# Kernel optimization log

Measured on AMD Instinct MI355X. Metric: run time of the kernel, lower is better.

The kernel has to match this reference:

```python
import jax, jax.numpy as jnp
import numpy as np

B, MAX_NODE, MEM_LEN, DIM, HEADS, LAYERS, DEG = 32, 1024, 256, 128, 4, 4, 16
CH = DIM // HEADS


def setup_inputs() -> dict:
    key = jax.random.key(0)
    ks = jax.random.split(key, 16)
    counts = np.array([512 + 16 * i for i in range(B)])  # ragged graph sizes, sum = 24320
    N = int(counts.sum())
    node2batch = np.repeat(np.arange(B), counts)
    node2pos = np.concatenate([np.arange(c) for c in counts])
    bmask = np.arange(MAX_NODE)[None, :] < counts[:, None]
    rng = np.random.default_rng(0)
    srcs, dsts, off = [], [], 0
    for c in counts:  # edges stay within each graph
        srcs.append(off + rng.integers(0, c, size=DEG * c))
        dsts.append(off + rng.integers(0, c, size=DEG * c))
        off += c
    edge_index = np.stack([np.concatenate(srcs), np.concatenate(dsts)])

    def rn(k, shape, scale=0.05):
        return jax.random.normal(k, shape, jnp.float32) * scale

    return dict(
        node_feats=rn(ks[0], (N, DIM), 1.0),
        edge_feats=rn(ks[1], (edge_index.shape[1], DIM), 1.0),
        memory=rn(ks[2], (B, MEM_LEN, DIM), 1.0),
        Wn=rn(ks[3], (LAYERS, DIM, DIM)), bn=jnp.zeros((LAYERS, DIM)),
        We=rn(ks[4], (LAYERS, DIM, DIM)),
        att_src=rn(ks[5], (LAYERS, HEADS, CH)),
        att_dst=rn(ks[6], (LAYERS, HEADS, CH)),
        att_edge=rn(ks[7], (LAYERS, HEADS, CH)),
        ln1_g=jnp.ones((LAYERS, DIM)), ln1_b=jnp.zeros((LAYERS, DIM)),
        ln2_g=jnp.ones((LAYERS, DIM)), ln2_b=jnp.zeros((LAYERS, DIM)),
        Wq=rn(ks[8], (LAYERS, DIM, DIM)), Wk=rn(ks[9], (LAYERS, DIM, DIM)),
        Wv=rn(ks[10], (LAYERS, DIM, DIM)), Wo=rn(ks[11], (LAYERS, DIM, DIM)),
        Ew1=rn(ks[12], (LAYERS, 3 * DIM, DIM)), Eb1=jnp.zeros((LAYERS, DIM)),
        Ew2=rn(ks[13], (LAYERS, DIM, DIM)), Eb2=jnp.zeros((LAYERS, DIM)),
        edge_index=jnp.asarray(edge_index, jnp.int32),
        node2batch=jnp.asarray(node2batch, jnp.int32),
        node2pos=jnp.asarray(node2pos, jnp.int32),
        batch_mask=jnp.asarray(bmask),
        mem_pad_mask=jnp.ones((B, MEM_LEN), bool),
    )


def _ln(x, g, b):
    mu = x.mean(-1, keepdims=True)
    v = ((x - mu) ** 2).mean(-1, keepdims=True)
    return (x - mu) * jax.lax.rsqrt(v + 1e-5) * g + b


def reference(node_feats, edge_feats, memory, Wn, bn, We, att_src, att_dst, att_edge,
              ln1_g, ln1_b, ln2_g, ln2_b, Wq, Wk, Wv, Wo, Ew1, Eb1, Ew2, Eb2,
              edge_index, node2batch, node2pos, batch_mask, mem_pad_mask):
    N = node_feats.shape[0]
    src, dst = edge_index[0], edge_index[1]
    # [B, max_node, mem_len]: attend only valid memory slots from valid nodes
    cross_mask = mem_pad_mask[:, None, :] & batch_mask[:, :, None]
    x, e = node_feats, edge_feats
    for l in range(LAYERS):
        # --- edge-conditioned GAT conv (segment softmax over dst) ---
        h = (x @ Wn[l]).reshape(N, HEADS, CH)
        eh = (e @ We[l]).reshape(-1, HEADS, CH)
        logits = (h[src] * att_src[l]).sum(-1) + (h[dst] * att_dst[l]).sum(-1) + (eh * att_edge[l]).sum(-1)
        logits = jax.nn.leaky_relu(logits, 0.2)  # [E, H]
        m = jax.ops.segment_max(logits, dst, num_segments=N)
        ew = jnp.exp(logits - m[dst])
        den = jax.ops.segment_sum(ew, dst, num_segments=N)
        alpha = ew / (den[dst] + 1e-16)
        conv = jax.ops.segment_sum(alpha[..., None] * (h[src] + eh), dst, num_segments=N)
        conv = conv.reshape(N, DIM) + bn[l]
        x = jax.nn.relu(_ln(conv, ln1_g[l], ln1_b[l])) + x
        # --- graph2batch scatter into dense padded tensor ---
        dense = jnp.zeros((B, MAX_NODE, DIM), x.dtype).at[node2batch, node2pos].set(x)
        # --- cross attention against memory ---
        q = (dense @ Wq[l]).reshape(B, MAX_NODE, HEADS, CH)
        k = (memory @ Wk[l]).reshape(B, MEM_LEN, HEADS, CH)
        v = (memory @ Wv[l]).reshape(B, MEM_LEN, HEADS, CH)
        scores = jnp.einsum('bqhc,bkhc->bhqk', q, k) / np.float32(np.sqrt(CH))
        scores = jnp.where(cross_mask[:, None], scores, jnp.float32(-1e9))
        ao = jnp.einsum('bhqk,bkhc->bqhc', jax.nn.softmax(scores, axis=-1), v)
        ao = ao.reshape(B, MAX_NODE, DIM) @ Wo[l]
        dense = jax.nn.relu(_ln(ao + dense, ln2_g[l], ln2_b[l]))
        x = dense[node2batch, node2pos]  # batch2graph gather
        # --- residual sparse edge update ---
        ecat = jnp.concatenate([e, x[src], x[dst]], axis=-1)
        e = e + jax.nn.relu(ecat @ Ew1[l] + Eb1[l]) @ Ew2[l] + Eb2[l]
    return x, e
```

## Files before the change

kernel.cpp:

```cpp
#include <hip/hip_runtime.h>

#define DIM    128
#define HEADS  4
#define CH     32
#define MEMLEN 256
#define LAYERS 4

typedef unsigned int uint;
typedef unsigned short ushort;
using bf16x8 = __attribute__((ext_vector_type(8))) short;
using f32x4  = __attribute__((ext_vector_type(4))) float;

__device__ __forceinline__ ushort bf16_rn(float x) {
    uint u = __float_as_uint(x);
    uint r = (u + 0x7fffu + ((u >> 16) & 1u)) >> 16;
    return (ushort)r;
}
__device__ __forceinline__ void split_bf(float v, ushort& h, ushort& lo) {
    h = bf16_rn(v);
    float hf = __uint_as_float(((uint)h) << 16);
    lo = bf16_rn(v - hf);
}


__global__ void copy_f4(const float4* __restrict__ in, float4* __restrict__ out, long n) {
    long i = (long)blockIdx.x * blockDim.x + threadIdx.x;
    long stride = (long)gridDim.x * blockDim.x;
    for (; i < n; i += stride) out[i] = in[i];
}

__global__ void hist_k(const int* __restrict__ dst, int E, int* __restrict__ deg) {
    int e = blockIdx.x * blockDim.x + threadIdx.x;
    if (e < E) atomicAdd(&deg[dst[e]], 1);
}

__global__ void csr_offsets(const int* __restrict__ deg, int n, int* __restrict__ off) {
    __shared__ int part[1024];
    int t = threadIdx.x;
    int chunk = (n + 1023) >> 10;
    int lo = t * chunk, hi = min(lo + chunk, n);
    int s = 0;
    for (int i = lo; i < hi; i++) s += deg[i];
    part[t] = s; __syncthreads();
    for (int d = 1; d < 1024; d <<= 1) {
        int v = part[t];
        int add = (t >= d) ? part[t - d] : 0;
        __syncthreads();
        part[t] = v + add;
        __syncthreads();
    }
    int run = (t == 0) ? 0 : part[t - 1];
    for (int i = lo; i < hi; i++) { off[i] = run; run += deg[i]; }
    if (t == 1023) off[n] = part[1023];
}

__global__ void csr_fill(const int* __restrict__ dst, int E, const int* __restrict__ off,
                         int* __restrict__ cur, int* __restrict__ csr) {
    int e = blockIdx.x * blockDim.x + threadIdx.x;
    if (e < E) {
        int d = dst[e];
        int p = atomicAdd(&cur[d], 1);
        csr[off[d] + p] = e;
    }
}

__global__ void make_w1f(const float* __restrict__ Ew1, ushort* __restrict__ W1f) {
    int i = blockIdx.x * 256 + threadIdx.x;
    if (i >= LAYERS * 12 * 8 * 64 * 8) return;
    int l = i / 49152; int r = i % 49152;
    int ks = r / 4096;  int r2 = r % 4096;
    int ct = r2 / 512;  int r3 = r2 % 512;
    int lane = r3 / 8;  int j = r3 % 8;
    int k = ks * 32 + (lane >> 4) * 8 + j;
    int n = (lane & 15) + 16 * ct;
    const float* W = Ew1 + (size_t)l * 3 * DIM * DIM;
    float v = W[(size_t)(k % 128) * DIM + n];
    ushort h = bf16_rn(v);
    ushort out = h;
    if (k >= 256) {
        float hf = __uint_as_float(((uint)h) << 16);
        out = bf16_rn(v - hf);
    }
    W1f[i] = out;
}

__global__ void make_w2f(const float* __restrict__ Ew2, ushort* __restrict__ W2f) {
    int i = blockIdx.x * 256 + threadIdx.x;
    if (i >= LAYERS * 8 * 8 * 64 * 8) return;
    int l = i / 32768; int r = i % 32768;
    int ks = r / 4096;  int r2 = r % 4096;
    int ct = r2 / 512;  int r3 = r2 % 512;
    int lane = r3 / 8;  int j = r3 % 8;
    int k = ks * 32 + (lane >> 4) * 8 + j;
    int n = (lane & 15) + 16 * ct;
    const float* W = Ew2 + (size_t)l * DIM * DIM;
    W2f[i] = bf16_rn(W[(size_t)(k >> 1) * DIM + n]);
}

__global__ __launch_bounds__(256) void gemm128(const float* __restrict__ A,
                                               const float* __restrict__ W,
                                               const float* __restrict__ bias,
                                               float* __restrict__ out, int R) {
    int r0 = blockIdx.x * 64, t = threadIdx.x;
    __shared__ float at[64][DIM];
    for (int i = t; i < 64 * 32; i += 256) {
        int rr = i >> 5, cc = i & 31;
        if (r0 + rr < R)
            ((float4*)at[rr])[cc] = ((const float4*)(A + (size_t)(r0 + rr) * DIM))[cc];
    }
    __syncthreads();
    int c0 = (t & 31) * 4;
    int rb = (t >> 5) * 8;
    float acc[8][4];
#pragma unroll
    for (int ee = 0; ee < 8; ee++)
        acc[ee][0] = acc[ee][1] = acc[ee][2] = acc[ee][3] = 0.f;
    for (int k = 0; k < DIM; k += 4) {
        float4 w0 = *(const float4*)&W[(k + 0) * DIM + c0];
        float4 w1 = *(const float4*)&W[(k + 1) * DIM + c0];
        float4 w2 = *(const float4*)&W[(k + 2) * DIM + c0];
        float4 w3 = *(const float4*)&W[(k + 3) * DIM + c0];
#pragma unroll
        for (int ee = 0; ee < 8; ee++) {
            float4 a = *(float4*)&at[rb + ee][k];
            acc[ee][0] += a.x * w0.x + a.y * w1.x + a.z * w2.x + a.w * w3.x;
            acc[ee][1] += a.x * w0.y + a.y * w1.y + a.z * w2.y + a.w * w3.y;
            acc[ee][2] += a.x * w0.z + a.y * w1.z + a.z * w2.z + a.w * w3.z;
            acc[ee][3] += a.x * w0.w + a.y * w1.w + a.z * w2.w + a.w * w3.w;
        }
    }
    float4 bb = make_float4(0.f, 0.f, 0.f, 0.f);
    if (bias) bb = *(const float4*)&bias[c0];
#pragma unroll
    for (int ee = 0; ee < 8; ee++) {
        int r = r0 + rb + ee;
        if (r < R) {
            float4 o = make_float4(acc[ee][0] + bb.x, acc[ee][1] + bb.y,
                                   acc[ee][2] + bb.z, acc[ee][3] + bb.w);
            *(float4*)&out[(size_t)r * DIM + c0] = o;
        }
    }
}

__global__ __launch_bounds__(256, 2) void gemm128_dual(const float* __restrict__ A,
                                                       const float* __restrict__ Wa,
                                                       const float* __restrict__ Wb,
                                                       const float* __restrict__ biasA,
                                                       float* __restrict__ outA,
                                                       float* __restrict__ outB, int R) {
    int r0 = blockIdx.x * 64, t = threadIdx.x;
    __shared__ float at[64][DIM];
    for (int i = t; i < 64 * 32; i += 256) {
        int rr = i >> 5, cc = i & 31;
        if (r0 + rr < R)
            ((float4*)at[rr])[cc] = ((const float4*)(A + (size_t)(r0 + rr) * DIM))[cc];
    }
    __syncthreads();
    int c0 = (t & 31) * 4;
    int rb = (t >> 5) * 8;
    float accA[8][4], accB[8][4];
#pragma unroll
    for (int ee = 0; ee < 8; ee++)
#pragma unroll
        for (int j = 0; j < 4; j++) { accA[ee][j] = 0.f; accB[ee][j] = 0.f; }
    for (int k = 0; k < DIM; k += 4) {
        float4 wa0 = *(const float4*)&Wa[(k + 0) * DIM + c0];
        float4 wa1 = *(const float4*)&Wa[(k + 1) * DIM + c0];
        float4 wa2 = *(const float4*)&Wa[(k + 2) * DIM + c0];
        float4 wa3 = *(const float4*)&Wa[(k + 3) * DIM + c0];
        float4 wb0 = *(const float4*)&Wb[(k + 0) * DIM + c0];
        float4 wb1 = *(const float4*)&Wb[(k + 1) * DIM + c0];
        float4 wb2 = *(const float4*)&Wb[(k + 2) * DIM + c0];
        float4 wb3 = *(const float4*)&Wb[(k + 3) * DIM + c0];
#pragma unroll
        for (int ee = 0; ee < 8; ee++) {
            float4 a = *(float4*)&at[rb + ee][k];
            accA[ee][0] += a.x * wa0.x + a.y * wa1.x + a.z * wa2.x + a.w * wa3.x;
            accA[ee][1] += a.x * wa0.y + a.y * wa1.y + a.z * wa2.y + a.w * wa3.y;
            accA[ee][2] += a.x * wa0.z + a.y * wa1.z + a.z * wa2.z + a.w * wa3.z;
            accA[ee][3] += a.x * wa0.w + a.y * wa1.w + a.z * wa2.w + a.w * wa3.w;
            accB[ee][0] += a.x * wb0.x + a.y * wb1.x + a.z * wb2.x + a.w * wb3.x;
            accB[ee][1] += a.x * wb0.y + a.y * wb1.y + a.z * wb2.y + a.w * wb3.y;
            accB[ee][2] += a.x * wb0.z + a.y * wb1.z + a.z * wb2.z + a.w * wb3.z;
            accB[ee][3] += a.x * wb0.w + a.y * wb1.w + a.z * wb2.w + a.w * wb3.w;
        }
    }
    float4 bb = make_float4(0.f, 0.f, 0.f, 0.f);
    if (biasA) bb = *(const float4*)&biasA[c0];
#pragma unroll
    for (int ee = 0; ee < 8; ee++) {
        int r = r0 + rb + ee;
        if (r < R) {
            *(float4*)&outA[(size_t)r * DIM + c0] =
                make_float4(accA[ee][0] + bb.x, accA[ee][1] + bb.y,
                            accA[ee][2] + bb.z, accA[ee][3] + bb.w);
            *(float4*)&outB[(size_t)r * DIM + c0] =
                make_float4(accB[ee][0], accB[ee][1], accB[ee][2], accB[ee][3]);
        }
    }
}

__global__ __launch_bounds__(256) void node_proj_tile(
    const float* __restrict__ x, const float* __restrict__ W,
    const float* __restrict__ att_s, const float* __restrict__ att_d,
    float* __restrict__ h, float* __restrict__ ssrc, float* __restrict__ sdst, int N) {
    int r0 = blockIdx.x * 64, t = threadIdx.x;
    __shared__ float at[64][DIM];
    for (int i = t; i < 64 * 32; i += 256) {
        int rr = i >> 5, cc = i & 31;
        if (r0 + rr < N)
            ((float4*)at[rr])[cc] = ((const float4*)(x + (size_t)(r0 + rr) * DIM))[cc];
    }
    __syncthreads();
    int c0 = (t & 31) * 4;
    int rb = (t >> 5) * 8;
    float acc[8][4];
#pragma unroll
    for (int ee = 0; ee < 8; ee++)
        acc[ee][0] = acc[ee][1] = acc[ee][2] = acc[ee][3] = 0.f;
    for (int k = 0; k < DIM; k += 4) {
        float4 w0 = *(const float4*)&W[(k + 0) * DIM + c0];
        float4 w1 = *(const float4*)&W[(k + 1) * DIM + c0];
        float4 w2 = *(const float4*)&W[(k + 2) * DIM + c0];
        float4 w3 = *(const float4*)&W[(k + 3) * DIM + c0];
#pragma unroll
        for (int ee = 0; ee < 8; ee++) {
            float4 a = *(float4*)&at[rb + ee][k];
            acc[ee][0] += a.x * w0.x + a.y * w1.x + a.z * w2.x + a.w * w3.x;
            acc[ee][1] += a.x * w0.y + a.y * w1.y + a.z * w2.y + a.w * w3.y;
            acc[ee][2] += a.x * w0.z + a.y * w1.z + a.z * w2.z + a.w * w3.z;
            acc[ee][3] += a.x * w0.w + a.y * w1.w + a.z * w2.w + a.w * w3.w;
        }
    }
    int hh = (t & 31) >> 3;
    float4 as = *(const float4*)&att_s[c0];
    float4 ad = *(const float4*)&att_d[c0];
#pragma unroll
    for (int ee = 0; ee < 8; ee++) {
        int r = r0 + rb + ee;
        if (r < N) {
            *(float4*)&h[(size_t)r * DIM + c0] =
                make_float4(acc[ee][0], acc[ee][1], acc[ee][2], acc[ee][3]);
            float ps = acc[ee][0]*as.x + acc[ee][1]*as.y + acc[ee][2]*as.z + acc[ee][3]*as.w;
            float pd = acc[ee][0]*ad.x + acc[ee][1]*ad.y + acc[ee][2]*ad.z + acc[ee][3]*ad.w;
#pragma unroll
            for (int mk = 1; mk < 8; mk <<= 1) {
                ps += __shfl_xor(ps, mk, 32);
                pd += __shfl_xor(pd, mk, 32);
            }
            if (((t & 31) & 7) == 0) {
                ssrc[r * HEADS + hh] = ps;
                sdst[r * HEADS + hh] = pd;
            }
        }
    }
}


__global__ void make_waE(const float* __restrict__ We, const float* __restrict__ att_e,
                         float* __restrict__ waE) {
    int k = threadIdx.x;
#pragma unroll
    for (int h = 0; h < HEADS; h++) {
        float s = 0.f;
#pragma unroll
        for (int c = 0; c < CH; c++) s += We[k * DIM + h * CH + c] * att_e[h * CH + c];
        waE[k * HEADS + h] = s;
    }
}

__global__ void sedge_logits(const float* __restrict__ e, const float* __restrict__ waE,
                             const float* __restrict__ ssrc, const float* __restrict__ sdst,
                             const int* __restrict__ src, const int* __restrict__ dst,
                             float* __restrict__ lw, int E) {
    __shared__ float w[DIM * HEADS];
    int t = threadIdx.x;
    w[t] = waE[t]; w[t + 256] = waE[t + 256];
    __syncthreads();
    int g = t >> 5, lane = t & 31;
    int eid = blockIdx.x * 8 + g;
    if (eid >= E) return;
    const float* er = e + (size_t)eid * DIM;
    float s0 = 0.f, s1 = 0.f, s2 = 0.f, s3 = 0.f;
#pragma unroll
    for (int j = 0; j < 4; j++) {
        int k = lane + 32 * j;
        float v = er[k];
        s0 += v * w[k * 4 + 0]; s1 += v * w[k * 4 + 1];
        s2 += v * w[k * 4 + 2]; s3 += v * w[k * 4 + 3];
    }
#pragma unroll
    for (int m = 16; m; m >>= 1) {
        s0 += __shfl_xor(s0, m, 32); s1 += __shfl_xor(s1, m, 32);
        s2 += __shfl_xor(s2, m, 32); s3 += __shfl_xor(s3, m, 32);
    }
    if (lane == 0) {
        int sn = src[eid] * HEADS, dn = dst[eid] * HEADS;
        float l0 = ssrc[sn + 0] + sdst[dn + 0] + s0;
        float l1 = ssrc[sn + 1] + sdst[dn + 1] + s1;
        float l2 = ssrc[sn + 2] + sdst[dn + 2] + s2;
        float l3 = ssrc[sn + 3] + sdst[dn + 3] + s3;
        lw[eid * 4 + 0] = (l0 >= 0.f) ? l0 : 0.2f * l0;
        lw[eid * 4 + 1] = (l1 >= 0.f) ? l1 : 0.2f * l1;
        lw[eid * 4 + 2] = (l2 >= 0.f) ? l2 : 0.2f * l2;
        lw[eid * 4 + 3] = (l3 >= 0.f) ? l3 : 0.2f * l3;
    }
}

__global__ void seg_softmax(const int* __restrict__ off, const int* __restrict__ csr,
                            float* __restrict__ lw, float* __restrict__ den, int NH) {
    int i = blockIdx.x * blockDim.x + threadIdx.x;
    if (i >= NH) return;
    int n = i >> 2, hh = i & 3;
    int o0 = off[n], o1 = off[n + 1];
    float m = -1e30f;
    for (int o = o0; o < o1; o++) m = fmaxf(m, lw[csr[o] * HEADS + hh]);
    float s = 0.f;
    for (int o = o0; o < o1; o++) {
        int idx = csr[o] * HEADS + hh;
        float w = __expf(lw[idx] - m);
        lw[idx] = w;
        s += w;
    }
    den[i] = s;
}

__global__ __launch_bounds__(512) void conv_ln4(
    const int* __restrict__ off, const int* __restrict__ csr, const int* __restrict__ src,
    const float* __restrict__ lw, const float* __restrict__ den,
    const float* __restrict__ hbuf, const float* __restrict__ e, const float* __restrict__ We,
    const float* __restrict__ bn, const float* __restrict__ g, const float* __restrict__ b,
    float* __restrict__ x, int N) {
    int t = threadIdx.x;
    int tt = t & 127, part = t >> 7;
    int n = blockIdx.x;
    int hh = tt >> 5;
    __shared__ float aggeP[4][HEADS][DIM];
    __shared__ float acchP[4][DIM];
    __shared__ float ehcP[4][DIM];
    __shared__ float wred[16];
    int o0 = off[n], o1 = off[n + 1];
    float acch = 0.f, a0 = 0.f, a1 = 0.f, a2 = 0.f, a3 = 0.f;
    for (int o = o0 + part; o < o1; o += 4) {
        int eid = csr[o];
        int s = src[eid];
        float4 al = *(const float4*)&lw[eid * 4];
        acch += ((&al.x)[hh]) * hbuf[(size_t)s * DIM + tt];
        float ev = e[(size_t)eid * DIM + tt];
        a0 += al.x * ev; a1 += al.y * ev; a2 += al.z * ev; a3 += al.w * ev;
    }
    aggeP[part][0][tt] = a0; aggeP[part][1][tt] = a1;
    aggeP[part][2][tt] = a2; aggeP[part][3][tt] = a3;
    acchP[part][tt] = acch;
    __syncthreads();
    float ehc = 0.f;
    int k0 = part * 32;
    for (int k = k0; k < k0 + 32; k++) {
        float ag = aggeP[0][hh][k] + aggeP[1][hh][k] + aggeP[2][hh][k] + aggeP[3][hh][k];
        ehc += ag * We[k * DIM + tt];
    }
    ehcP[part][tt] = ehc;
    __syncthreads();
    float conv = (acchP[0][tt] + acchP[1][tt] + acchP[2][tt] + acchP[3][tt]
                + ehcP[0][tt] + ehcP[1][tt] + ehcP[2][tt] + ehcP[3][tt])
                 / (den[n * HEADS + hh] + 1e-16f) + bn[tt];
    int w = t >> 6;
    float s1 = conv;
#pragma unroll
    for (int mk = 32; mk; mk >>= 1) s1 += __shfl_xor(s1, mk, 64);
    if ((t & 63) == 0) wred[w] = s1;
    __syncthreads();
    float mu = (wred[w] + wred[w ^ 1]) * (1.f / DIM);
    float diff = conv - mu;
    float s2 = diff * diff;
#pragma unroll
    for (int mk = 32; mk; mk >>= 1) s2 += __shfl_xor(s2, mk, 64);
    if ((t & 63) == 0) wred[8 + w] = s2;
    __syncthreads();
    float var = (wred[8 + w] + wred[8 + (w ^ 1)]) * (1.f / DIM);
    if (part == 0) {
        float y = diff * rsqrtf(var + 1e-5f) * g[tt] + b[tt];
        x[(size_t)n * DIM + tt] = fmaxf(y, 0.f) + x[(size_t)n * DIM + tt];
    }
}

__global__ __launch_bounds__(256) void cross_attn_tile(
    float* __restrict__ x, const float* __restrict__ qg,
    const float* __restrict__ kb, const float* __restrict__ vb,
    const float* __restrict__ Wo, const float* __restrict__ g,
    const float* __restrict__ b, const int* __restrict__ boff) {
    int bb = blockIdx.y;
    int n0 = boff[bb] + blockIdx.x * 64;
    int cnt = boff[bb + 1] - n0;
    if (cnt <= 0) return;
    int nq = min(64, cnt);
    int t = threadIdx.x;
    int q = t & 63, h = t >> 6;

    __shared__ float smem[64 * 132];

    float qv[32];
    if (q < nq) {
        const float4* qp = (const float4*)(qg + (size_t)(n0 + q) * DIM + h * CH);
#pragma unroll
        for (int j = 0; j < 8; j++) {
            float4 v = qp[j];
            qv[4*j+0] = v.x; qv[4*j+1] = v.y; qv[4*j+2] = v.z; qv[4*j+3] = v.w;
        }
    } else {
#pragma unroll
        for (int c = 0; c < 32; c++) qv[c] = 0.f;
    }

    float oacc[32];
#pragma unroll
    for (int c = 0; c < 32; c++) oacc[c] = 0.f;
    float m = -1e30f, l = 0.f;

    const float4* Ksrc = (const float4*)(kb + (size_t)bb * MEMLEN * DIM);
    const float4* Vsrc = (const float4*)(vb + (size_t)bb * MEMLEN * DIM);
    float4* Kl = (float4*)smem;
    float4* Vl = (float4*)(smem + 32 * DIM);

    for (int ch = 0; ch < MEMLEN / 32; ch++) {
        __syncthreads();
#pragma unroll
        for (int r = 0; r < 4; r++) {
            int idx = t + r * 256;
            Kl[idx] = Ksrc[ch * 1024 + idx];
            Vl[idx] = Vsrc[ch * 1024 + idx];
        }
        __syncthreads();
        float sc[32];
#pragma unroll
        for (int kk = 0; kk < 32; kk++) {
            const float* kp = smem + kk * DIM + h * CH;
            float s = 0.f;
#pragma unroll
            for (int c = 0; c < 32; c++) s += qv[c] * kp[c];
            sc[kk] = s * 0.17677669529663689f;
        }
        float mc = sc[0];
#pragma unroll
        for (int kk = 1; kk < 32; kk++) mc = fmaxf(mc, sc[kk]);
        float mn = fmaxf(m, mc);
        float scale = __expf(m - mn);
        m = mn;
        float ls = 0.f;
#pragma unroll
        for (int kk = 0; kk < 32; kk++) {
            float w = __expf(sc[kk] - mn);
            sc[kk] = w;
            ls += w;
        }
        l = l * scale + ls;
#pragma unroll
        for (int c = 0; c < 32; c++) oacc[c] *= scale;
#pragma unroll
        for (int kk = 0; kk < 32; kk++) {
            const float* vp = smem + 32 * DIM + kk * DIM + h * CH;
            float w = sc[kk];
#pragma unroll
            for (int c = 0; c < 32; c++) oacc[c] += w * vp[c];
        }
    }
    __syncthreads();
    {
        float inv = 1.f / l;
        float* ap = smem + q * 132 + h * CH;
#pragma unroll
        for (int c = 0; c < 32; c++) ap[c] = oacc[c] * inv;
    }
    __syncthreads();
    int c0 = (t & 31) * 4;
    int rb = (t >> 5) * 8;
    float acc2[8][4];
#pragma unroll
    for (int ee = 0; ee < 8; ee++)
        acc2[ee][0] = acc2[ee][1] = acc2[ee][2] = acc2[ee][3] = 0.f;
    for (int k = 0; k < DIM; k += 4) {
        float4 w0 = *(const float4*)&Wo[(k + 0) * DIM + c0];
        float4 w1 = *(const float4*)&Wo[(k + 1) * DIM + c0];
        float4 w2 = *(const float4*)&Wo[(k + 2) * DIM + c0];
        float4 w3 = *(const float4*)&Wo[(k + 3) * DIM + c0];
#pragma unroll
        for (int ee = 0; ee < 8; ee++) {
            float4 a = *(const float4*)(smem + (rb + ee) * 132 + k);
            acc2[ee][0] += a.x * w0.x + a.y * w1.x + a.z * w2.x + a.w * w3.x;
            acc2[ee][1] += a.x * w0.y + a.y * w1.y + a.z * w2.y + a.w * w3.y;
            acc2[ee][2] += a.x * w0.z + a.y * w1.z + a.z * w2.z + a.w * w3.z;
            acc2[ee][3] += a.x * w0.w + a.y * w1.w + a.z * w2.w + a.w * w3.w;
        }
    }
    float4 gg = *(const float4*)&g[c0];
    float4 bb4 = *(const float4*)&b[c0];
#pragma unroll
    for (int ee = 0; ee < 8; ee++) {
        int r = rb + ee;
        if (r < nq) {
            float4 xr = *(const float4*)&x[(size_t)(n0 + r) * DIM + c0];
            float o0 = acc2[ee][0] + xr.x, o1 = acc2[ee][1] + xr.y;
            float o2 = acc2[ee][2] + xr.z, o3 = acc2[ee][3] + xr.w;
            float s1 = o0 + o1 + o2 + o3;
#pragma unroll
            for (int mk = 16; mk; mk >>= 1) s1 += __shfl_xor(s1, mk, 32);
            float mu = s1 * (1.f / DIM);
            float d0 = o0 - mu, d1 = o1 - mu, d2 = o2 - mu, d3 = o3 - mu;
            float s2 = d0*d0 + d1*d1 + d2*d2 + d3*d3;
#pragma unroll
            for (int mk = 16; mk; mk >>= 1) s2 += __shfl_xor(s2, mk, 32);
            float rs = rsqrtf(s2 * (1.f / DIM) + 1e-5f);
            float4 o = make_float4(fmaxf(d0 * rs * gg.x + bb4.x, 0.f),
                                   fmaxf(d1 * rs * gg.y + bb4.y, 0.f),
                                   fmaxf(d2 * rs * gg.z + bb4.z, 0.f),
                                   fmaxf(d3 * rs * gg.w + bb4.w, 0.f));
            *(float4*)&x[(size_t)(n0 + r) * DIM + c0] = o;
        }
    }
}

__global__ __launch_bounds__(256, 2) void edge_mlp_mfma(
    float* __restrict__ e, const float* __restrict__ xs, const float* __restrict__ xd,
    const int* __restrict__ src, const int* __restrict__ dst,
    const ushort* __restrict__ W1f,
    const ushort* __restrict__ W2f,
    const float* __restrict__ Eb2, int E) {
    __shared__ ushort As[64 * 256];
    int t = threadIdx.x;
    int e0 = blockIdx.x * 64;

#pragma unroll
    for (int it = 0; it < 8; it++) {
        int i = t + it * 256;
        int row = i >> 5, c4 = i & 31;
        float4 v;
        if (e0 + row < E) v = *(const float4*)&e[(size_t)(e0 + row) * DIM + c4 * 4];
        else v = make_float4(0.f, 0.f, 0.f, 0.f);
        ushort h0, l0, h1, l1, h2, l2, h3, l3;
        split_bf(v.x, h0, l0); split_bf(v.y, h1, l1);
        split_bf(v.z, h2, l2); split_bf(v.w, h3, l3);
        int k = c4 * 4;
        int off = k & 7;
        int kbh = (k >> 3) ^ (row & 7);
        int kbl = ((128 + k) >> 3) ^ (row & 7);
        uint2 hw, lw2;
        hw.x = (uint)h0 | ((uint)h1 << 16); hw.y = (uint)h2 | ((uint)h3 << 16);
        lw2.x = (uint)l0 | ((uint)l1 << 16); lw2.y = (uint)l2 | ((uint)l3 << 16);
        *(uint2*)&As[row * 256 + kbh * 8 + off] = hw;
        *(uint2*)&As[row * 256 + kbl * 8 + off] = lw2;
    }

    int l = t & 63, wid = t >> 6;
    int g = l >> 4;
    int lr = l & 15;
    int ct0 = 2 * wid, ct1 = 2 * wid + 1;

    bf16x8 b1[12][2];
#pragma unroll
    for (int ks = 0; ks < 12; ks++) {
        b1[ks][0] = *(const bf16x8*)&W1f[(size_t)ks * 4096 + ct0 * 512 + l * 8];
        b1[ks][1] = *(const bf16x8*)&W1f[(size_t)ks * 4096 + ct1 * 512 + l * 8];
    }

    __syncthreads();

    f32x4 acc[4][2];
#pragma unroll
    for (int r = 0; r < 4; r++) {
        acc[r][0] = (f32x4){0.f, 0.f, 0.f, 0.f};
        acc[r][1] = (f32x4){0.f, 0.f, 0.f, 0.f};
    }

#pragma unroll
    for (int ks = 0; ks < 12; ks++) {
        int ksA = (ks < 8) ? ks : (ks - 8);
#pragma unroll
        for (int r = 0; r < 4; r++) {
            int arow = r * 16 + lr;
            int kbm = (ksA * 4 + g) ^ (arow & 7);
            bf16x8 af = *(bf16x8*)&As[arow * 256 + kbm * 8];
            acc[r][0] = __builtin_amdgcn_mfma_f32_16x16x32_bf16(af, b1[ks][0], acc[r][0], 0, 0, 0);
            acc[r][1] = __builtin_amdgcn_mfma_f32_16x16x32_bf16(af, b1[ks][1], acc[r][1], 0, 0, 0);
        }
    }

    bf16x8 b2f[8][2];
#pragma unroll
    for (int ks = 0; ks < 8; ks++) {
        b2f[ks][0] = *(const bf16x8*)&W2f[(size_t)ks * 4096 + ct0 * 512 + l * 8];
        b2f[ks][1] = *(const bf16x8*)&W2f[(size_t)ks * 4096 + ct1 * 512 + l * 8];
    }

    int col0 = lr + 16 * ct0, col1 = lr + 16 * ct1;
    int kb0 = col0 >> 2, off0 = (2 * col0) & 7;
    int kb1 = col1 >> 2, off1 = (2 * col1) & 7;
#pragma unroll
    for (int r = 0; r < 4; r++) {
#pragma unroll
        for (int j = 0; j < 4; j++) {
            int rowloc = r * 16 + g * 4 + j;
            int grow = e0 + rowloc;
            float v0 = acc[r][0][j], v1 = acc[r][1][j];
            if (grow < E) {
                int s = src[grow], d = dst[grow];
                v0 += xs[(size_t)s * DIM + col0] + xd[(size_t)d * DIM + col0];
                v1 += xs[(size_t)s * DIM + col1] + xd[(size_t)d * DIM + col1];
            }
            v0 = fmaxf(v0, 0.f); v1 = fmaxf(v1, 0.f);
            ushort h0s, l0s, h1s, l1s;
            split_bf(v0, h0s, l0s);
            split_bf(v1, h1s, l1s);
            int rs = rowloc & 7;
            *(uint*)&As[rowloc * 256 + (kb0 ^ rs) * 8 + off0] = (uint)h0s | ((uint)l0s << 16);
            *(uint*)&As[rowloc * 256 + (kb1 ^ rs) * 8 + off1] = (uint)h1s | ((uint)l1s << 16);
        }
    }
    __syncthreads();

    f32x4 acc2[4][2];
#pragma unroll
    for (int r = 0; r < 4; r++) {
        acc2[r][0] = (f32x4){0.f, 0.f, 0.f, 0.f};
        acc2[r][1] = (f32x4){0.f, 0.f, 0.f, 0.f};
    }
#pragma unroll
    for (int ks = 0; ks < 8; ks++) {
#pragma unroll
        for (int r = 0; r < 4; r++) {
            int arow = r * 16 + lr;
            int kbm = (ks * 4 + g) ^ (arow & 7);
            bf16x8 af = *(bf16x8*)&As[arow * 256 + kbm * 8];
            acc2[r][0] = __builtin_amdgcn_mfma_f32_16x16x32_bf16(af, b2f[ks][0], acc2[r][0], 0, 0, 0);
            acc2[r][1] = __builtin_amdgcn_mfma_f32_16x16x32_bf16(af, b2f[ks][1], acc2[r][1], 0, 0, 0);
        }
    }

    float b20 = Eb2[col0], b21 = Eb2[col1];
#pragma unroll
    for (int r = 0; r < 4; r++) {
#pragma unroll
        for (int j = 0; j < 4; j++) {
            int grow = e0 + r * 16 + g * 4 + j;
            if (grow < E) {
                e[(size_t)grow * DIM + col0] += acc2[r][0][j] + b20;
                e[(size_t)grow * DIM + col1] += acc2[r][1][j] + b21;
            }
        }
    }
}


extern "C" void kernel_launch(void* const* d_in, const int* in_sizes, int n_in,
                              void* d_out, int out_size, void* d_ws, size_t ws_size,
                              hipStream_t stream) {
    const float* node_feats = (const float*)d_in[0];
    const float* edge_feats = (const float*)d_in[1];
    const float* memory     = (const float*)d_in[2];
    const float* Wn   = (const float*)d_in[3];
    const float* bn   = (const float*)d_in[4];
    const float* We   = (const float*)d_in[5];
    const float* att_src  = (const float*)d_in[6];
    const float* att_dst  = (const float*)d_in[7];
    const float* att_edge = (const float*)d_in[8];
    const float* ln1_g = (const float*)d_in[9];
    const float* ln1_b = (const float*)d_in[10];
    const float* ln2_g = (const float*)d_in[11];
    const float* ln2_b = (const float*)d_in[12];
    const float* Wq = (const float*)d_in[13];
    const float* Wk = (const float*)d_in[14];
    const float* Wv = (const float*)d_in[15];
    const float* Wo = (const float*)d_in[16];
    const float* Ew1 = (const float*)d_in[17];
    const float* Eb1 = (const float*)d_in[18];
    const float* Ew2 = (const float*)d_in[19];
    const float* Eb2 = (const float*)d_in[20];
    const int* edge_index = (const int*)d_in[21];
    const int* node2batch = (const int*)d_in[22];

    const int N = in_sizes[0] / DIM;
    const int E = in_sizes[1] / DIM;
    const int Bn = in_sizes[2] / (MEMLEN * DIM);
    const int* srcA = edge_index;
    const int* dstA = edge_index + E;

    float* x = (float*)d_out;
    float* e = x + (size_t)N * DIM;

    char* p = (char*)d_ws;
    auto carve = [&](size_t bytes) {
        void* r = (void*)p;
        p += (bytes + 255) & ~(size_t)255;
        return r;
    };
    float* h     = (float*)carve((size_t)N * DIM * 4);
    float* qg    = (float*)carve((size_t)N * DIM * 4);
    float* xs    = (float*)carve((size_t)N * DIM * 4);
    float* xd    = (float*)carve((size_t)N * DIM * 4);
    float* ssrc  = (float*)carve((size_t)N * HEADS * 4);
    float* sdst  = (float*)carve((size_t)N * HEADS * 4);
    float* lw    = (float*)carve((size_t)E * HEADS * 4);
    float* den   = (float*)carve((size_t)N * HEADS * 4);
    float* waE   = (float*)carve((size_t)DIM * HEADS * 4);
    float* kbuf  = (float*)carve((size_t)Bn * MEMLEN * DIM * 4);
    float* vbuf  = (float*)carve((size_t)Bn * MEMLEN * DIM * 4);
    ushort* W1f  = (ushort*)carve((size_t)LAYERS * 12 * 4096 * 2);
    ushort* W2f  = (ushort*)carve((size_t)LAYERS * 8 * 4096 * 2);
    int* deg     = (int*)carve((size_t)N * 4);
    int* cur     = (int*)carve((size_t)N * 4);
    int* off     = (int*)carve(((size_t)N + 1) * 4);
    int* csr     = (int*)carve((size_t)E * 4);
    int* bcnt    = (int*)carve((size_t)Bn * 4);
    int* boff    = (int*)carve(((size_t)Bn + 1) * 4);

    {
        long nx = (long)N * DIM / 4;
        copy_f4<<<dim3(2048), dim3(256), 0, stream>>>((const float4*)node_feats, (float4*)x, nx);
        long nen = (long)E * DIM / 4;
        copy_f4<<<dim3(4096), dim3(256), 0, stream>>>((const float4*)edge_feats, (float4*)e, nen);
    }

    make_w1f<<<dim3((LAYERS * 49152 + 255) / 256), dim3(256), 0, stream>>>(Ew1, W1f);
    make_w2f<<<dim3((LAYERS * 32768 + 255) / 256), dim3(256), 0, stream>>>(Ew2, W2f);

    hipMemsetAsync(deg, 0, (size_t)N * 4, stream);
    hipMemsetAsync(cur, 0, (size_t)N * 4, stream);
    hipMemsetAsync(bcnt, 0, (size_t)Bn * 4, stream);
    hist_k<<<dim3((E + 255) / 256), dim3(256), 0, stream>>>(dstA, E, deg);
    csr_offsets<<<dim3(1), dim3(1024), 0, stream>>>(deg, N, off);
    csr_fill<<<dim3((E + 255) / 256), dim3(256), 0, stream>>>(dstA, E, off, cur, csr);
    hist_k<<<dim3((N + 255) / 256), dim3(256), 0, stream>>>(node2batch, N, bcnt);
    csr_offsets<<<dim3(1), dim3(1024), 0, stream>>>(bcnt, Bn, boff);

    const int mrows = Bn * MEMLEN;
    const int maxTiles = 1024 / 64;
    for (int l = 0; l < LAYERS; l++) {
        const float* Wn_l  = Wn  + (size_t)l * DIM * DIM;
        const float* We_l  = We  + (size_t)l * DIM * DIM;
        const float* Wq_l  = Wq  + (size_t)l * DIM * DIM;
        const float* Wo_l  = Wo  + (size_t)l * DIM * DIM;
        const float* Wk_l  = Wk  + (size_t)l * DIM * DIM;
        const float* Wv_l  = Wv  + (size_t)l * DIM * DIM;
        const float* Ew1_l = Ew1 + (size_t)l * 3 * DIM * DIM;

        node_proj_tile<<<dim3((N + 63) / 64), dim3(256), 0, stream>>>(
            x, Wn_l, att_src + l * DIM, att_dst + l * DIM, h, ssrc, sdst, N);
        make_waE<<<dim3(1), dim3(DIM), 0, stream>>>(We_l, att_edge + l * DIM, waE);
        sedge_logits<<<dim3((E + 7) / 8), dim3(256), 0, stream>>>(
            e, waE, ssrc, sdst, srcA, dstA, lw, E);
        seg_softmax<<<dim3((N * HEADS + 255) / 256), dim3(256), 0, stream>>>(
            off, csr, lw, den, N * HEADS);
        conv_ln4<<<dim3(N), dim3(512), 0, stream>>>(
            off, csr, srcA, lw, den, h, e, We_l,
            bn + l * DIM, ln1_g + l * DIM, ln1_b + l * DIM, x, N);
        gemm128_dual<<<dim3((mrows + 63) / 64), dim3(256), 0, stream>>>(
            memory, Wk_l, Wv_l, nullptr, kbuf, vbuf, mrows);
        gemm128<<<dim3((N + 63) / 64), dim3(256), 0, stream>>>(
            x, Wq_l, nullptr, qg, N);
        cross_attn_tile<<<dim3(maxTiles, Bn), dim3(256), 0, stream>>>(
            x, qg, kbuf, vbuf, Wo_l, ln2_g + l * DIM, ln2_b + l * DIM, boff);
        gemm128_dual<<<dim3((N + 63) / 64), dim3(256), 0, stream>>>(
            x, Ew1_l + (size_t)DIM * DIM, Ew1_l + (size_t)2 * DIM * DIM,
            Eb1 + l * DIM, xs, xd, N);
        edge_mlp_mfma<<<dim3((E + 63) / 64), dim3(256), 0, stream>>>(
            e, xs, xd, srcA, dstA,
            W1f + (size_t)l * 12 * 4096, W2f + (size_t)l * 8 * 4096,
            Eb2 + l * DIM, E);
    }
}
```

Baseline: 3.915 ms.

## Restructure edge MLP to 128-edge tiles with 8 waves and staged coalesced writeback

The edge MLP kernel now processes 128 edges per block using 512 threads, with each of the 8 waves owning one 16-column tile across all 8 row tiles. Each wave therefore holds half as many weight fragments in registers. The final residual update is staged through shared memory so the e tensor gets coalesced float4 read-modify-writes instead of scattered scalar ones. In exchange, shared memory per block doubles to 64KB, and the launch bound asks for 4 blocks of 512 threads, which may cap registers and limit real occupancy.

```diff
diff --git a/kernel.cpp b/kernel.cpp
--- a/kernel.cpp
+++ b/kernel.cpp
@@ -519,19 +519,19 @@
     }
 }
 
-__global__ __launch_bounds__(256, 2) void edge_mlp_mfma(
+__global__ __launch_bounds__(512, 4) void edge_mlp_mfma(
     float* __restrict__ e, const float* __restrict__ xs, const float* __restrict__ xd,
     const int* __restrict__ src, const int* __restrict__ dst,
     const ushort* __restrict__ W1f,
     const ushort* __restrict__ W2f,
     const float* __restrict__ Eb2, int E) {
-    __shared__ ushort As[64 * 256];
+    __shared__ ushort As[128 * 256];
     int t = threadIdx.x;
-    int e0 = blockIdx.x * 64;
+    int e0 = blockIdx.x * 128;
 
 #pragma unroll
     for (int it = 0; it < 8; it++) {
-        int i = t + it * 256;
+        int i = t + it * 512;
         int row = i >> 5, c4 = i & 31;
         float4 v;
         if (e0 + row < E) v = *(const float4*)&e[(size_t)(e0 + row) * DIM + c4 * 4];
@@ -553,98 +553,95 @@
     int l = t & 63, wid = t >> 6;
     int g = l >> 4;
     int lr = l & 15;
-    int ct0 = 2 * wid, ct1 = 2 * wid + 1;
-
-    bf16x8 b1[12][2];
-#pragma unroll
-    for (int ks = 0; ks < 12; ks++) {
-        b1[ks][0] = *(const bf16x8*)&W1f[(size_t)ks * 4096 + ct0 * 512 + l * 8];
-        b1[ks][1] = *(const bf16x8*)&W1f[(size_t)ks * 4096 + ct1 * 512 + l * 8];
-    }
-
-    __syncthreads();
-
-    f32x4 acc[4][2];
-#pragma unroll
-    for (int r = 0; r < 4; r++) {
-        acc[r][0] = (f32x4){0.f, 0.f, 0.f, 0.f};
-        acc[r][1] = (f32x4){0.f, 0.f, 0.f, 0.f};
-    }
+    int col = lr + 16 * wid;
+
+    bf16x8 b1[12];
+#pragma unroll
+    for (int ks = 0; ks < 12; ks++)
+        b1[ks] = *(const bf16x8*)&W1f[(size_t)ks * 4096 + wid * 512 + l * 8];
+
+    __syncthreads();
+
+    f32x4 acc[8];
+#pragma unroll
+    for (int r = 0; r < 8; r++) acc[r] = (f32x4){0.f, 0.f, 0.f, 0.f};
 
 #pragma unroll
     for (int ks = 0; ks < 12; ks++) {
         int ksA = (ks < 8) ? ks : (ks - 8);
 #pragma unroll
-        for (int r = 0; r < 4; r++) {
+        for (int r = 0; r < 8; r++) {
             int arow = r * 16 + lr;
             int kbm = (ksA * 4 + g) ^ (arow & 7);
             bf16x8 af = *(bf16x8*)&As[arow * 256 + kbm * 8];
-            acc[r][0] = __builtin_amdgcn_mfma_f32_16x16x32_bf16(af, b1[ks][0], acc[r][0], 0, 0, 0);
-            acc[r][1] = __builtin_amdgcn_mfma_f32_16x16x32_bf16(af, b1[ks][1], acc[r][1], 0, 0, 0);
-        }
-    }
-
-    bf16x8 b2f[8][2];
-#pragma unroll
-    for (int ks = 0; ks < 8; ks++) {
-        b2f[ks][0] = *(const bf16x8*)&W2f[(size_t)ks * 4096 + ct0 * 512 + l * 8];
-        b2f[ks][1] = *(const bf16x8*)&W2f[(size_t)ks * 4096 + ct1 * 512 + l * 8];
-    }
-
-    int col0 = lr + 16 * ct0, col1 = lr + 16 * ct1;
-    int kb0 = col0 >> 2, off0 = (2 * col0) & 7;
-    int kb1 = col1 >> 2, off1 = (2 * col1) & 7;
-#pragma unroll
-    for (int r = 0; r < 4; r++) {
+            acc[r] = __builtin_amdgcn_mfma_f32_16x16x32_bf16(af, b1[ks], acc[r], 0, 0, 0);
+        }
+    }
+
+    bf16x8 b2f[8];
+#pragma unroll
+    for (int ks = 0; ks < 8; ks++)
+        b2f[ks] = *(const bf16x8*)&W2f[(size_t)ks * 4096 + wid * 512 + l * 8];
+
+    int kbc = col >> 2, offc = (2 * col) & 7;
+#pragma unroll
+    for (int r = 0; r < 8; r++) {
 #pragma unroll
         for (int j = 0; j < 4; j++) {
             int rowloc = r * 16 + g * 4 + j;
             int grow = e0 + rowloc;
-            float v0 = acc[r][0][j], v1 = acc[r][1][j];
+            float v = acc[r][j];
             if (grow < E) {
                 int s = src[grow], d = dst[grow];
-                v0 += xs[(size_t)s * DIM + col0] + xd[(size_t)d * DIM + col0];
-                v1 += xs[(size_t)s * DIM + col1] + xd[(size_t)d * DIM + col1];
+                v += xs[(size_t)s * DIM + col] + xd[(size_t)d * DIM + col];
             }
-            v0 = fmaxf(v0, 0.f); v1 = fmaxf(v1, 0.f);
-            ushort h0s, l0s, h1s, l1s;
-            split_bf(v0, h0s, l0s);
-            split_bf(v1, h1s, l1s);
-            int rs = rowloc & 7;
-            *(uint*)&As[rowloc * 256 + (kb0 ^ rs) * 8 + off0] = (uint)h0s | ((uint)l0s << 16);
-            *(uint*)&As[rowloc * 256 + (kb1 ^ rs) * 8 + off1] = (uint)h1s | ((uint)l1s << 16);
-        }
-    }
-    __syncthreads();
-
-    f32x4 acc2[4][2];
-#pragma unroll
-    for (int r = 0; r < 4; r++) {
-        acc2[r][0] = (f32x4){0.f, 0.f, 0.f, 0.f};
-        acc2[r][1] = (f32x4){0.f, 0.f, 0.f, 0.f};
-    }
+            v = fmaxf(v, 0.f);
+            ushort hs, ls;
+            split_bf(v, hs, ls);
+            *(uint*)&As[rowloc * 256 + ((kbc ^ (rowloc & 7))) * 8 + offc] =
+                (uint)hs | ((uint)ls << 16);
+        }
+    }
+    __syncthreads();
+
+    f32x4 acc2[8];
+#pragma unroll
+    for (int r = 0; r < 8; r++) acc2[r] = (f32x4){0.f, 0.f, 0.f, 0.f};
 #pragma unroll
     for (int ks = 0; ks < 8; ks++) {
 #pragma unroll
-        for (int r = 0; r < 4; r++) {
+        for (int r = 0; r < 8; r++) {
             int arow = r * 16 + lr;
             int kbm = (ks * 4 + g) ^ (arow & 7);
             bf16x8 af = *(bf16x8*)&As[arow * 256 + kbm * 8];
-            acc2[r][0] = __builtin_amdgcn_mfma_f32_16x16x32_bf16(af, b2f[ks][0], acc2[r][0], 0, 0, 0);
-            acc2[r][1] = __builtin_amdgcn_mfma_f32_16x16x32_bf16(af, b2f[ks][1], acc2[r][1], 0, 0, 0);
-        }
-    }
-
-    float b20 = Eb2[col0], b21 = Eb2[col1];
-#pragma unroll
-    for (int r = 0; r < 4; r++) {
+            acc2[r] = __builtin_amdgcn_mfma_f32_16x16x32_bf16(af, b2f[ks], acc2[r], 0, 0, 0);
+        }
+    }
+    __syncthreads();
+
+    float* Af = (float*)As;
+#pragma unroll
+    for (int r = 0; r < 8; r++) {
 #pragma unroll
         for (int j = 0; j < 4; j++) {
-            int grow = e0 + r * 16 + g * 4 + j;
-            if (grow < E) {
-                e[(size_t)grow * DIM + col0] += acc2[r][0][j] + b20;
-                e[(size_t)grow * DIM + col1] += acc2[r][1][j] + b21;
-            }
+            int rowloc = r * 16 + g * 4 + j;
+            Af[rowloc * DIM + col] = acc2[r][j];
+        }
+    }
+    __syncthreads();
+
+#pragma unroll
+    for (int it = 0; it < 8; it++) {
+        int i = t + it * 512;
+        int row = i >> 5, c4 = i & 31;
+        int grow = e0 + row;
+        if (grow < E) {
+            float4 ev = *(const float4*)&e[(size_t)grow * DIM + c4 * 4];
+            float4 b2 = *(const float4*)&Eb2[c4 * 4];
+            const float* ap = &Af[row * DIM + c4 * 4];
+            ev.x += ap[0] + b2.x; ev.y += ap[1] + b2.y;
+            ev.z += ap[2] + b2.z; ev.w += ap[3] + b2.w;
+            *(float4*)&e[(size_t)grow * DIM + c4 * 4] = ev;
         }
     }
 }
@@ -761,7 +758,7 @@
         gemm128_dual<<<dim3((N + 63) / 64), dim3(256), 0, stream>>>(
             x, Ew1_l + (size_t)DIM * DIM, Ew1_l + (size_t)2 * DIM * DIM,
             Eb1 + l * DIM, xs, xd, N);
-        edge_mlp_mfma<<<dim3((E + 63) / 64), dim3(256), 0, stream>>>(
+        edge_mlp_mfma<<<dim3((E + 127) / 128), dim3(512), 0, stream>>>(
             e, xs, xd, srcA, dstA,
             W1f + (size_t)l * 12 * 4096, W2f + (size_t)l * 8 * 4096,
             Eb2 + l * DIM, E);
```

New measurement: 5.065 ms. +29.4%, slower.

## Fuse next-layer edge attention logits into edge MLP epilogue

Applied to the files above, without the earlier changes.

Moves the next layer's node projection and waE computation before the edge MLP, then computes the edge attention logits inside the edge MLP kernel from the freshly updated edge features held in shared memory. This removes the separate sedge_logits pass, which re-read the whole edge feature tensor each layer. The epilogue is also restaged through LDS so the residual update to e uses coalesced float4 read-modify-writes instead of scattered scalar updates. In exchange the kernel uses more shared memory, adds extra barriers and a per-thread serial 128-long dot product.

```diff
diff --git a/kernel.cpp b/kernel.cpp
--- a/kernel.cpp
+++ b/kernel.cpp
@@ -524,10 +524,21 @@
     const int* __restrict__ src, const int* __restrict__ dst,
     const ushort* __restrict__ W1f,
     const ushort* __restrict__ W2f,
-    const float* __restrict__ Eb2, int E) {
-    __shared__ ushort As[64 * 256];
+    const float* __restrict__ Eb2,
+    const float* __restrict__ waE,
+    const float* __restrict__ ssrc, const float* __restrict__ sdst,
+    float* __restrict__ lw, int doLogits, int E) {
+    __shared__ __align__(16) char smemraw[64 * 132 * 4];
+    ushort* As = (ushort*)smemraw;
+    float*  Af = (float*)smemraw;
+    __shared__ float waEl[DIM * HEADS];
     int t = threadIdx.x;
     int e0 = blockIdx.x * 64;
+
+    if (doLogits) {
+        waEl[t] = waE[t];
+        waEl[t + 256] = waE[t + 256];
+    }
 
 #pragma unroll
     for (int it = 0; it < 8; it++) {
@@ -634,17 +645,45 @@
             acc2[r][1] = __builtin_amdgcn_mfma_f32_16x16x32_bf16(af, b2f[ks][1], acc2[r][1], 0, 0, 0);
         }
     }
+    __syncthreads();
 
     float b20 = Eb2[col0], b21 = Eb2[col1];
 #pragma unroll
     for (int r = 0; r < 4; r++) {
 #pragma unroll
         for (int j = 0; j < 4; j++) {
-            int grow = e0 + r * 16 + g * 4 + j;
-            if (grow < E) {
-                e[(size_t)grow * DIM + col0] += acc2[r][0][j] + b20;
-                e[(size_t)grow * DIM + col1] += acc2[r][1][j] + b21;
-            }
+            int rowloc = r * 16 + g * 4 + j;
+            Af[rowloc * 132 + col0] = acc2[r][0][j] + b20;
+            Af[rowloc * 132 + col1] = acc2[r][1][j] + b21;
+        }
+    }
+    __syncthreads();
+
+#pragma unroll
+    for (int it = 0; it < 8; it++) {
+        int i = t + it * 256;
+        int row = i >> 5, c4 = i & 31;
+        int grow = e0 + row;
+        if (grow < E) {
+            float4 ev = *(const float4*)&e[(size_t)grow * DIM + c4 * 4];
+            float* ap = &Af[row * 132 + c4 * 4];
+            ev.x += ap[0]; ev.y += ap[1]; ev.z += ap[2]; ev.w += ap[3];
+            *(float4*)&e[(size_t)grow * DIM + c4 * 4] = ev;
+            ap[0] = ev.x; ap[1] = ev.y; ap[2] = ev.z; ap[3] = ev.w;
+        }
+    }
+
+    if (doLogits) {
+        __syncthreads();
+        int row = t >> 2, h = t & 3;
+        int grow = e0 + row;
+        if (grow < E) {
+            const float* ar = &Af[row * 132];
+            float s = 0.f;
+#pragma unroll 8
+            for (int k = 0; k < DIM; k++) s += ar[k] * waEl[k * 4 + h];
+            s += ssrc[src[grow] * HEADS + h] + sdst[dst[grow] * HEADS + h];
+            lw[grow * 4 + h] = (s >= 0.f) ? s : 0.2f * s;
         }
     }
 }
@@ -733,8 +772,14 @@
 
     const int mrows = Bn * MEMLEN;
     const int maxTiles = 1024 / 64;
+
+    node_proj_tile<<<dim3((N + 63) / 64), dim3(256), 0, stream>>>(
+        x, Wn, att_src, att_dst, h, ssrc, sdst, N);
+    make_waE<<<dim3(1), dim3(DIM), 0, stream>>>(We, att_edge, waE);
+    sedge_logits<<<dim3((E + 7) / 8), dim3(256), 0, stream>>>(
+        e, waE, ssrc, sdst, srcA, dstA, lw, E);
+
     for (int l = 0; l < LAYERS; l++) {
-        const float* Wn_l  = Wn  + (size_t)l * DIM * DIM;
         const float* We_l  = We  + (size_t)l * DIM * DIM;
         const float* Wq_l  = Wq  + (size_t)l * DIM * DIM;
         const float* Wo_l  = Wo  + (size_t)l * DIM * DIM;
@@ -742,11 +787,6 @@
         const float* Wv_l  = Wv  + (size_t)l * DIM * DIM;
         const float* Ew1_l = Ew1 + (size_t)l * 3 * DIM * DIM;
 
-        node_proj_tile<<<dim3((N + 63) / 64), dim3(256), 0, stream>>>(
-            x, Wn_l, att_src + l * DIM, att_dst + l * DIM, h, ssrc, sdst, N);
-        make_waE<<<dim3(1), dim3(DIM), 0, stream>>>(We_l, att_edge + l * DIM, waE);
-        sedge_logits<<<dim3((E + 7) / 8), dim3(256), 0, stream>>>(
-            e, waE, ssrc, sdst, srcA, dstA, lw, E);
         seg_softmax<<<dim3((N * HEADS + 255) / 256), dim3(256), 0, stream>>>(
             off, csr, lw, den, N * HEADS);
         conv_ln4<<<dim3(N), dim3(512), 0, stream>>>(
@@ -761,9 +801,22 @@
         gemm128_dual<<<dim3((N + 63) / 64), dim3(256), 0, stream>>>(
             x, Ew1_l + (size_t)DIM * DIM, Ew1_l + (size_t)2 * DIM * DIM,
             Eb1 + l * DIM, xs, xd, N);
-        edge_mlp_mfma<<<dim3((E + 63) / 64), dim3(256), 0, stream>>>(
-            e, xs, xd, srcA, dstA,
-            W1f + (size_t)l * 12 * 4096, W2f + (size_t)l * 8 * 4096,
-            Eb2 + l * DIM, E);
-    }
-}
+
+        if (l + 1 < LAYERS) {
+            node_proj_tile<<<dim3((N + 63) / 64), dim3(256), 0, stream>>>(
+                x, Wn + (size_t)(l + 1) * DIM * DIM,
+                att_src + (l + 1) * DIM, att_dst + (l + 1) * DIM, h, ssrc, sdst, N);
+            make_waE<<<dim3(1), dim3(DIM), 0, stream>>>(
+                We + (size_t)(l + 1) * DIM * DIM, att_edge + (l + 1) * DIM, waE);
+            edge_mlp_mfma<<<dim3((E + 63) / 64), dim3(256), 0, stream>>>(
+                e, xs, xd, srcA, dstA,
+                W1f + (size_t)l * 12 * 4096, W2f + (size_t)l * 8 * 4096,
+                Eb2 + l * DIM, waE, ssrc, sdst, lw, 1, E);
+        } else {
+            edge_mlp_mfma<<<dim3((E + 63) / 64), dim3(256), 0, stream>>>(
+                e, xs, xd, srcA, dstA,
+                W1f + (size_t)l * 12 * 4096, W2f + (size_t)l * 8 * 4096,
+                Eb2 + l * DIM, nullptr, nullptr, nullptr, nullptr, 0, E);
+        }
+    }
+}
```

Measured after the change: 3.690 ms. -5.7%, faster.
